# Performance work log

Measured on AMD Instinct MI355X. Metric: run time of the kernel, lower is better.

## Reference

```python
import jax, jax.numpy as jnp
import numpy as np

NEG_SLOPE = 0.2  # GATConv default negative_slope
EPS = 1e-12      # F.normalize default eps


def chain_edges(n):
    # reading-order chain (i-1<->i) plus one self-loop per node
    # (PyG GATConv removes existing self-loops then adds them for all nodes)
    f = np.arange(n - 1)
    src = np.concatenate([f, f + 1, np.arange(n)])
    dst = np.concatenate([f + 1, f, np.arange(n)])
    return jnp.asarray(src, dtype=jnp.int32), jnp.asarray(dst, dtype=jnp.int32)


def gat_conv(x, W, att_src, att_dst, bias, src, dst, n):
    h = x @ W                                   # [n, d]
    a_s = h @ att_src                           # [n]
    a_d = h @ att_dst                           # [n]
    e = jax.nn.leaky_relu(a_s[src] + a_d[dst], NEG_SLOPE)      # [E]
    e_max = jax.ops.segment_max(e, dst, num_segments=n)
    ex = jnp.exp(e - e_max[dst])
    denom = jax.ops.segment_sum(ex, dst, num_segments=n)
    alpha = ex / denom[dst]                     # softmax over incoming edges
    out = jax.ops.segment_sum(alpha[:, None] * h[src], dst, num_segments=n)
    return out + bias


def cosine_cost(t1, t2):
    n1 = t1 / jnp.maximum(jnp.linalg.norm(t1, axis=-1, keepdims=True), EPS)
    n2 = t2 / jnp.maximum(jnp.linalg.norm(t2, axis=-1, keepdims=True), EPS)
    return 1.0 - jnp.abs(jnp.einsum('bnd,bmd->bnm', n1, n2))   # [B, N, M]


def lsa_square(cost):
    # Jonker-Volgenant style Hungarian (e-maxx), square numpy float64 matrix.
    # Returns row index assigned to each column (optimal assignment).
    n = cost.shape[0]
    INF = np.inf
    u = np.zeros(n + 1)
    v = np.zeros(n + 1)
    p = np.zeros(n + 1, dtype=np.int64)
    way = np.zeros(n + 1, dtype=np.int64)
    for i in range(1, n + 1):
        p[0] = i
        j0 = 0
        minv = np.full(n + 1, INF)
        used = np.zeros(n + 1, dtype=bool)
        while True:
            used[j0] = True
            i0 = p[j0]
            free = ~used[1:]
            cur = cost[i0 - 1] - u[i0] - v[1:]
            mv = minv[1:]
            better = free & (cur < mv)
            mv[better] = cur[better]
            way[1:][better] = j0
            masked = np.where(free, mv, INF)
            j1 = int(np.argmin(masked)) + 1
            delta = masked[j1 - 1]
            u[p[used]] += delta
            v[used] -= delta
            mv[free] -= delta
            j0 = j1
            if p[j0] == 0:
                break
        while j0 != 0:
            j1 = way[j0]
            p[j0] = p[j1]
            j0 = j1
    return p[1:] - 1


def setup_inputs() -> dict:
    key = jax.random.key(0)
    k1, k2, k3, k4, k5 = jax.random.split(key, 5)
    B, N, M, D = 32, 320, 320, 512
    dense_t1 = jax.random.normal(k1, (B, N, D), jnp.float32)
    dense_t2 = jax.random.normal(k2, (B, M, D), jnp.float32)
    t1_mask = jnp.ones((B, N), dtype=bool)
    t2_mask = jnp.ones((B, M), dtype=bool)
    W = jax.random.normal(k3, (D, D), jnp.float32) / np.float32(np.sqrt(D))
    att_src = jax.random.normal(k4, (D,), jnp.float32) / np.float32(np.sqrt(D))
    att_dst = jax.random.normal(k5, (D,), jnp.float32) / np.float32(np.sqrt(D))
    bias = jnp.zeros((D,), jnp.float32)
    return {"dense_t1": dense_t1, "dense_t2": dense_t2, "t1_mask": t1_mask,
            "t2_mask": t2_mask, "W": W, "att_src": att_src, "att_dst": att_dst,
            "bias": bias}


def reference(dense_t1, dense_t2, t1_mask, t2_mask, W, att_src, att_dst, bias):
    B, N, _ = dense_t1.shape
    M = dense_t2.shape[1]
    src1, dst1 = chain_edges(N)
    src2, dst2 = chain_edges(M)
    # Message passing is computed as in the original module; note the original
    # hungarian_distance ignores h1/h2 and matches on PRE-context features.
    _h1 = jax.vmap(lambda x: gat_conv(x, W, att_src, att_dst, bias, src1, dst1, N))(dense_t1)
    _h2 = jax.vmap(lambda x: gat_conv(x, W, att_src, att_dst, bias, src2, dst2, M))(dense_t2)
    cost = cosine_cost(dense_t1, dense_t2)                     # [B, N, M]
    cost_np = np.asarray(jax.device_get(cost)).astype(np.float64)
    rows = np.stack([lsa_square(cost_np[b]) for b in range(B)])  # [B, M]
    cols = np.arange(M)[None, :].repeat(B, 0)
    matched = cost[np.arange(B)[:, None], rows, cols]          # [B, M]
    return matched.mean(axis=1)                                # [B]
```

## Files before the change

kernel.cpp:

```cpp
#include <hip/hip_runtime.h>
#include <hip/hip_bf16.h>
#include <math.h>

#define NB 32
#define NN 320
#define ND 512
#define KC 5
#define FINF 1e30f

__global__ __launch_bounds__(64) void norm_kernel(const float* __restrict__ t,
                                                  float* __restrict__ s) {
    int row = blockIdx.x;
    const float4* p = (const float4*)(t + (size_t)row * ND);
    int tid = threadIdx.x;
    float4 a = p[tid];
    float4 b = p[tid + 64];
    float sum = a.x*a.x + a.y*a.y + a.z*a.z + a.w*a.w
              + b.x*b.x + b.y*b.y + b.z*b.z + b.w*b.w;
#pragma unroll
    for (int off = 32; off; off >>= 1) sum += __shfl_down(sum, off, 64);
    if (tid == 0) s[row] = 1.0f / fmaxf(sqrtf(sum), 1e-12f);
}

__global__ __launch_bounds__(256) void cost_kernel(const float* __restrict__ t1,
                                                   const float* __restrict__ t2,
                                                   const float* __restrict__ s1,
                                                   const float* __restrict__ s2,
                                                   float* __restrict__ cost) {
    int b    = blockIdx.y;
    int tile = blockIdx.x;
    int bm0  = (tile / 5) * 64;
    int bn0  = (tile % 5) * 64;
    const float* A  = t1 + (size_t)b * NN * ND;
    const float* Bm = t2 + (size_t)b * NN * ND;
    float* C = cost + (size_t)b * NN * NN;

    __shared__ float As[16][64];
    __shared__ float Bs[16][64];

    int tid = threadIdx.x;
    int tx = tid & 15, ty = tid >> 4;
    int sm = tid >> 2;
    int skg = (tid & 3) * 4;

    float acc[4][4] = {};

    for (int k0 = 0; k0 < ND; k0 += 16) {
        float4 av = *(const float4*)(A  + (size_t)(bm0 + sm) * ND + k0 + skg);
        float4 bv = *(const float4*)(Bm + (size_t)(bn0 + sm) * ND + k0 + skg);
        __syncthreads();
        As[skg+0][sm] = av.x; As[skg+1][sm] = av.y; As[skg+2][sm] = av.z; As[skg+3][sm] = av.w;
        Bs[skg+0][sm] = bv.x; Bs[skg+1][sm] = bv.y; Bs[skg+2][sm] = bv.z; Bs[skg+3][sm] = bv.w;
        __syncthreads();
#pragma unroll
        for (int k = 0; k < 16; ++k) {
            float4 a4 = *(const float4*)&As[k][ty * 4];
            float4 b4 = *(const float4*)&Bs[k][tx * 4];
            float ar[4] = {a4.x, a4.y, a4.z, a4.w};
            float br[4] = {b4.x, b4.y, b4.z, b4.w};
#pragma unroll
            for (int r = 0; r < 4; ++r)
#pragma unroll
                for (int c = 0; c < 4; ++c)
                    acc[r][c] += ar[r] * br[c];
        }
    }

    float s2v[4];
#pragma unroll
    for (int c = 0; c < 4; ++c) s2v[c] = s2[b * NN + bn0 + tx * 4 + c];
#pragma unroll
    for (int r = 0; r < 4; ++r) {
        int gm = bm0 + ty * 4 + r;
        float s1v = s1[b * NN + gm];
        float4 o;
        o.x = 1.0f - fabsf(acc[r][0] * s1v * s2v[0]);
        o.y = 1.0f - fabsf(acc[r][1] * s1v * s2v[1]);
        o.z = 1.0f - fabsf(acc[r][2] * s1v * s2v[2]);
        o.w = 1.0f - fabsf(acc[r][3] * s1v * s2v[3]);
        *(float4*)(C + (size_t)gm * NN + bn0 + tx * 4) = o;
    }
}

template<int CTRL>
__device__ __forceinline__ float dpp_fmin(float x) {
    int xi = __float_as_int(x);
    int oi = __builtin_amdgcn_update_dpp(xi, xi, CTRL, 0xf, 0xf, false);
    return fminf(x, __int_as_float(oi));
}
__device__ __forceinline__ float wave_fmin_bcast(float x) {
    x = dpp_fmin<0x111>(x);
    x = dpp_fmin<0x112>(x);
    x = dpp_fmin<0x114>(x);
    x = dpp_fmin<0x118>(x);
    x = dpp_fmin<0x142>(x);
    x = dpp_fmin<0x143>(x);
    return __int_as_float(__builtin_amdgcn_readlane(__float_as_int(x), 63));
}

__global__ __launch_bounds__(64) void lsa_kernel(const float* __restrict__ cost_all,
                                                 float* __restrict__ out) {
    int b = blockIdx.x;
    const float* __restrict__ C = cost_all + (size_t)b * NN * NN;
    int t = threadIdx.x;

    __shared__ float u_lds[NN + 1];
    __shared__ int   p_lds[NN + 1];
    __shared__ int   way_lds[NN + 1];
    __shared__ int   assigned[NN + 1];

    for (int j = t; j <= NN; j += 64) {
        u_lds[j] = 0.0f; p_lds[j] = 0; way_lds[j] = 0; assigned[j] = 0;
    }

    float v[KC];
#pragma unroll
    for (int k = 0; k < KC; ++k) v[k] = FINF;
#pragma unroll 4
    for (int i = 0; i < NN; ++i) {
        const float* row = C + (size_t)i * NN + t;
#pragma unroll
        for (int k = 0; k < KC; ++k) v[k] = fminf(v[k], row[64 * k]);
    }

    int preg[KC];
#pragma unroll
    for (int k = 0; k < KC; ++k) preg[k] = 0;

    {
        float f[KC], fn[KC];
#pragma unroll
        for (int k = 0; k < KC; ++k) f[k] = C[t + 64 * k];
        for (int r = 0; r < NN; ++r) {
            if (r + 1 < NN) {
                const float* nrow = C + (size_t)(r + 1) * NN + t;
#pragma unroll
                for (int k = 0; k < KC; ++k) fn[k] = nrow[64 * k];
            }
            float bv = FINF; int bk = 0;
#pragma unroll
            for (int k = 0; k < KC; ++k) {
                float m = f[k] - v[k];
                if (m < bv) { bv = m; bk = k; }
            }
            float wmin = wave_fmin_bcast(bv);
            unsigned long long mask = __ballot(bv == wmin);
            int lsel = (int)__builtin_ctzll(mask);
            int jm = __builtin_amdgcn_readlane(t + 1 + (bk << 6), lsel);
            if (t == 0) u_lds[r + 1] = wmin;
            int jz = jm - 1, l2 = jz & 63, wh = jz >> 6;
            int pv = 0;
#pragma unroll
            for (int k = 0; k < KC; ++k) {
                int c = __builtin_amdgcn_readlane(preg[k], l2);
                if (wh == k) pv = c;
            }
            if (pv == 0) {
                if (t == 0) { p_lds[jm] = r + 1; assigned[r + 1] = 1; }
                if (l2 == t) {
#pragma unroll
                    for (int k = 0; k < KC; ++k) if (wh == k) preg[k] = r + 1;
                }
            }
            if (r + 1 < NN) {
#pragma unroll
                for (int k = 0; k < KC; ++k) f[k] = fn[k];
            }
        }
    }

    for (int r = 0; r < NN; ++r) {
        if (assigned[r + 1]) continue;
        const int i_row = r + 1;
        if (t == 0) p_lds[0] = i_row;
        float D[KC]; bool used[KC];
#pragma unroll
        for (int k = 0; k < KC; ++k) { D[k] = FINF; used[k] = false; }
        int i0 = i_row, curj = 0;
        float Dcur = 0.0f, minVal = 0.0f;
        int j1 = 0;
        for (;;) {
            const float* row = C + (size_t)(i0 - 1) * NN + t;
            float ui0 = u_lds[i0];
            float f[KC];
#pragma unroll
            for (int k = 0; k < KC; ++k) f[k] = row[64 * k];
            float s = Dcur - ui0;
            float bv = FINF; int bk = 0;
#pragma unroll
            for (int k = 0; k < KC; ++k) {
                if (!used[k]) {
                    float rr = f[k] + (s - v[k]);
                    if (rr < D[k]) { D[k] = rr; way_lds[t + 1 + (k << 6)] = curj; }
                    if (D[k] < bv) { bv = D[k]; bk = k; }
                }
            }
            float wmin = wave_fmin_bcast(bv);
            unsigned long long mask = __ballot(bv == wmin);
            int lsel = (int)__builtin_ctzll(mask);
            j1 = __builtin_amdgcn_readlane(t + 1 + (bk << 6), lsel);
            Dcur = wmin;
            int jz = j1 - 1, l2 = jz & 63, wh = jz >> 6;
            int pv = 0;
#pragma unroll
            for (int k = 0; k < KC; ++k) {
                int c = __builtin_amdgcn_readlane(preg[k], l2);
                if (wh == k) pv = c;
            }
            if (pv == 0) { minVal = wmin; break; }
            {
                bool me = (l2 == t);
#pragma unroll
                for (int k = 0; k < KC; ++k) if (me && wh == k) used[k] = true;
            }
            i0 = pv; curj = j1;
        }
#pragma unroll
        for (int k = 0; k < KC; ++k) {
            if (used[k]) {
                float adj = minVal - D[k];
                v[k] -= adj;
                u_lds[preg[k]] += adj;
            }
        }
        if (t == 0) {
            u_lds[i_row] += minVal;
            int j = j1;
            while (j != 0) { int jp = way_lds[j]; p_lds[j] = p_lds[jp]; j = jp; }
        }
#pragma unroll
        for (int k = 0; k < KC; ++k) preg[k] = p_lds[t + 1 + (k << 6)];
    }

    double sum = 0.0;
#pragma unroll
    for (int k = 0; k < KC; ++k) {
        int c = t + 64 * k;
        int i = p_lds[c + 1] - 1;
        sum += (double)C[(size_t)i * NN + c];
    }
#pragma unroll
    for (int off = 32; off; off >>= 1) sum += __shfl_down(sum, off, 64);
    if (t == 0) out[b] = (float)(sum / (double)NN);
}

extern "C" void kernel_launch(void* const* d_in, const int* in_sizes, int n_in,
                              void* d_out, int out_size, void* d_ws, size_t ws_size,
                              hipStream_t stream) {
    (void)in_sizes; (void)n_in; (void)out_size; (void)ws_size;
    const float* t1 = (const float*)d_in[0];
    const float* t2 = (const float*)d_in[1];
    float* out = (float*)d_out;

    float* s1   = (float*)d_ws;
    float* s2   = s1 + NB * NN;
    float* cost = s2 + NB * NN;

    norm_kernel<<<NB * NN, 64, 0, stream>>>(t1, s1);
    norm_kernel<<<NB * NN, 64, 0, stream>>>(t2, s2);
    cost_kernel<<<dim3(25, NB), 256, 0, stream>>>(t1, t2, s1, s2, cost);
    lsa_kernel<<<NB, 64, 0, stream>>>(cost, out);
}
```

Baseline: 2.916 ms.

## Add auction-style augmenting row reduction before Hungarian shortest-path phase

Inserts two passes of augmenting row reduction (JV-style) after the column/row reduction init. Each pass finds the two smallest reduced costs per unassigned row, assigns it and may evict the current owner while adjusting column duals. This shrinks the number of rows left for the costlier shortest augmenting path search. It also adds bounds guards, step limits and __syncthreads barriers. These add overhead and may hide correctness issues by falling back when indices are invalid.

```diff
diff --git a/kernel.cpp b/kernel.cpp
--- a/kernel.cpp
+++ b/kernel.cpp
@@ -112,6 +112,7 @@
     for (int j = t; j <= NN; j += 64) {
         u_lds[j] = 0.0f; p_lds[j] = 0; way_lds[j] = 0; assigned[j] = 0;
     }
+    __syncthreads();
 
     float v[KC];
 #pragma unroll
@@ -145,7 +146,7 @@
             }
             float wmin = wave_fmin_bcast(bv);
             unsigned long long mask = __ballot(bv == wmin);
-            int lsel = (int)__builtin_ctzll(mask);
+            int lsel = mask ? (int)__builtin_ctzll(mask) : 0;
             int jm = __builtin_amdgcn_readlane(t + 1 + (bk << 6), lsel);
             if (t == 0) u_lds[r + 1] = wmin;
             int jz = jm - 1, l2 = jz & 63, wh = jz >> 6;
@@ -167,6 +168,60 @@
                 for (int k = 0; k < KC; ++k) f[k] = fn[k];
             }
         }
+    }
+    __syncthreads();
+
+    for (int pass = 0; pass < 2; ++pass) {
+        int budget = 2 * NN;
+        for (int r0 = 1; r0 <= NN; ++r0) {
+            if (assigned[r0]) continue;
+            int i = r0;
+            while (i != 0 && --budget >= 0) {
+                const float* row = C + (size_t)(i - 1) * NN + t;
+                float lm1 = FINF, lm2 = FINF; int bk = 0;
+#pragma unroll
+                for (int k = 0; k < KC; ++k) {
+                    float m = row[64 * k] - v[k];
+                    if (m < lm1) { lm2 = lm1; lm1 = m; bk = k; }
+                    else         { lm2 = fminf(lm2, m); }
+                }
+                float wm1 = wave_fmin_bcast(lm1);
+                unsigned long long mask = __ballot(lm1 == wm1);
+                if (!mask) break;
+                int lsel = (int)__builtin_ctzll(mask);
+                int j1 = __builtin_amdgcn_readlane(t + 1 + (bk << 6), lsel);
+                float wm2 = wave_fmin_bcast((t == lsel) ? lm2 : lm1);
+                float adj = wm2 - wm1;
+                if (j1 < 1 || j1 > NN) break;
+                int jz = j1 - 1, l2 = jz & 63, wh = jz >> 6;
+                int pv = 0;
+#pragma unroll
+                for (int k = 0; k < KC; ++k) {
+                    int c = __builtin_amdgcn_readlane(preg[k], l2);
+                    if (wh == k) pv = c;
+                }
+                if (pv < 0 || pv > NN) pv = 0;
+                if (t == 0) u_lds[i] = wm2;
+                if (pv == 0 || adj > 0.0f) {
+                    if (t == 0) {
+                        p_lds[j1] = i; assigned[i] = 1;
+                        if (pv) assigned[pv] = 0;
+                    }
+                    if (t == l2) {
+#pragma unroll
+                        for (int k = 0; k < KC; ++k) if (wh == k) {
+                            preg[k] = i;
+                            v[k] -= adj;
+                        }
+                    }
+                    i = pv;
+                } else {
+                    i = 0;
+                }
+                __syncthreads();
+            }
+        }
+        __syncthreads();
     }
 
     for (int r = 0; r < NN; ++r) {
@@ -179,7 +234,8 @@
         int i0 = i_row, curj = 0;
         float Dcur = 0.0f, minVal = 0.0f;
         int j1 = 0;
-        for (;;) {
+        bool okpath = false;
+        for (int step = 0; step <= NN; ++step) {
             const float* row = C + (size_t)(i0 - 1) * NN + t;
             float ui0 = u_lds[i0];
             float f[KC];
@@ -197,8 +253,9 @@
             }
             float wmin = wave_fmin_bcast(bv);
             unsigned long long mask = __ballot(bv == wmin);
-            int lsel = (int)__builtin_ctzll(mask);
+            int lsel = mask ? (int)__builtin_ctzll(mask) : 0;
             j1 = __builtin_amdgcn_readlane(t + 1 + (bk << 6), lsel);
+            if (j1 < 1 || j1 > NN) break;
             Dcur = wmin;
             int jz = j1 - 1, l2 = jz & 63, wh = jz >> 6;
             int pv = 0;
@@ -207,7 +264,7 @@
                 int c = __builtin_amdgcn_readlane(preg[k], l2);
                 if (wh == k) pv = c;
             }
-            if (pv == 0) { minVal = wmin; break; }
+            if (pv <= 0 || pv > NN) { minVal = wmin; okpath = true; break; }
             {
                 bool me = (l2 == t);
 #pragma unroll
@@ -215,29 +272,35 @@
             }
             i0 = pv; curj = j1;
         }
-#pragma unroll
-        for (int k = 0; k < KC; ++k) {
-            if (used[k]) {
-                float adj = minVal - D[k];
-                v[k] -= adj;
-                u_lds[preg[k]] += adj;
-            }
-        }
-        if (t == 0) {
-            u_lds[i_row] += minVal;
-            int j = j1;
-            while (j != 0) { int jp = way_lds[j]; p_lds[j] = p_lds[jp]; j = jp; }
-        }
+        if (okpath) {
+#pragma unroll
+            for (int k = 0; k < KC; ++k) {
+                if (used[k]) {
+                    float adj = minVal - D[k];
+                    v[k] -= adj;
+                    u_lds[preg[k]] += adj;
+                }
+            }
+            if (t == 0) {
+                u_lds[i_row] += minVal;
+                int j = j1;
+                int guard = NN + 1;
+                while (j != 0 && --guard >= 0) { int jp = way_lds[j]; p_lds[j] = p_lds[jp]; j = jp; }
+            }
+        }
+        __syncthreads();
 #pragma unroll
         for (int k = 0; k < KC; ++k) preg[k] = p_lds[t + 1 + (k << 6)];
     }
+    __syncthreads();
 
     double sum = 0.0;
 #pragma unroll
     for (int k = 0; k < KC; ++k) {
         int c = t + 64 * k;
-        int i = p_lds[c + 1] - 1;
-        sum += (double)C[(size_t)i * NN + c];
+        int p = p_lds[c + 1];
+        if (p < 1 || p > NN) p = c + 1;
+        sum += (double)C[(size_t)(p - 1) * NN + c];
     }
 #pragma unroll
     for (int off = 32; off; off >>= 1) sum += __shfl_down(sum, off, 64);
```

Measured after the change: 2.782 ms. 4.6% less time.
